# Kernel tuning notes

Measured on AMD Instinct MI355X. Metric: run time of the kernel, lower is better.

The kernel has to match this reference:

```python
import jax, jax.numpy as jnp
import numpy as np
import math

S, B, D = 1024, 8, 1024
H = 16
DK = D // H
F = 4096
EPS = 1e-5


def _layernorm(x, g, b):
    m = jnp.mean(x, axis=-1, keepdims=True)
    v = jnp.mean(jnp.square(x - m), axis=-1, keepdims=True)
    return (x - m) * jax.lax.rsqrt(v + EPS) * g + b


def setup_inputs() -> dict:
    key = jax.random.key(0)
    ks = jax.random.split(key, 16)
    sc = 0.02
    inp = {
        "src": jax.random.normal(ks[0], (S, B, D), dtype=jnp.float32),
        "pos": jax.random.normal(ks[1], (S, B, D), dtype=jnp.float32),
        "Wq": jax.random.normal(ks[2], (D, D), dtype=jnp.float32) * sc,
        "bq": jnp.zeros((D,), dtype=jnp.float32),
        "Wk": jax.random.normal(ks[3], (D, D), dtype=jnp.float32) * sc,
        "bk": jnp.zeros((D,), dtype=jnp.float32),
        "Wv": jax.random.normal(ks[4], (D, D), dtype=jnp.float32) * sc,
        "bv": jnp.zeros((D,), dtype=jnp.float32),
        "Wo": jax.random.normal(ks[5], (D, D), dtype=jnp.float32) * sc,
        "bo": jnp.zeros((D,), dtype=jnp.float32),
        "W1": jax.random.normal(ks[6], (D, F), dtype=jnp.float32) * sc,
        "b1": jnp.zeros((F,), dtype=jnp.float32),
        "W2": jax.random.normal(ks[7], (F, D), dtype=jnp.float32) * sc,
        "b2": jnp.zeros((D,), dtype=jnp.float32),
        "g1": jnp.ones((D,), dtype=jnp.float32),
        "be1": jnp.zeros((D,), dtype=jnp.float32),
        "g2": jnp.ones((D,), dtype=jnp.float32),
        "be2": jnp.zeros((D,), dtype=jnp.float32),
    }
    return inp


def reference(src, pos, Wq, bq, Wk, bk, Wv, bv, Wo, bo, W1, b1, W2, b2, g1, be1, g2, be2):
    # post-norm encoder layer; dropout = identity (eval mode)
    qk_in = src + pos                      # q = k = src + pos, value = src
    # to batch-first [B, S, D]
    qb = jnp.transpose(qk_in, (1, 0, 2))
    vb = jnp.transpose(src, (1, 0, 2))

    def split_heads(x):                    # [B,S,D] -> [B,H,S,DK]
        return jnp.transpose(x.reshape(B, S, H, DK), (0, 2, 1, 3))

    q = split_heads(qb @ Wq + bq)
    k = split_heads(qb @ Wk + bk)
    v = split_heads(vb @ Wv + bv)

    scores = jnp.einsum('bhqd,bhkd->bhqk', q, k) / math.sqrt(DK)
    attn = jax.nn.softmax(scores, axis=-1)             # [B,H,S,S]
    ctx = jnp.einsum('bhqk,bhkd->bhqd', attn, v)       # [B,H,S,DK]
    ctx = jnp.transpose(ctx, (0, 2, 1, 3)).reshape(B, S, D)
    attn_out = ctx @ Wo + bo                           # [B,S,D]
    attn_out = jnp.transpose(attn_out, (1, 0, 2))      # back to [S,B,D]

    x = _layernorm(src + attn_out, g1, be1)
    ffn = jax.nn.relu(x @ W1 + b1) @ W2 + b2
    out = _layernorm(x + ffn, g2, be2)
    return out, attn
```

## Files before the change

kernel.cpp:

```cpp
#include <hip/hip_runtime.h>
#include <stdint.h>

#define S_ 1024
#define B_ 8
#define D_ 1024
#define H_ 16
#define DK_ 64
#define F_ 4096
#define EPS_ 1e-5f

typedef __bf16 bf16_t;
typedef __attribute__((ext_vector_type(8))) __bf16 bf16x8;
typedef __attribute__((ext_vector_type(4))) __bf16 bf16x4;
typedef __attribute__((ext_vector_type(4))) float f32x4;

#define GLD16(gp, lp) __builtin_amdgcn_global_load_lds( \
    (__attribute__((address_space(1))) void*)(void*)(gp), \
    (__attribute__((address_space(3))) void*)(lp), 16, 0, 0)

#define BAR() __builtin_amdgcn_s_barrier()
#define SB0() __builtin_amdgcn_sched_barrier(0)
#define LG0() do { asm volatile("s_waitcnt lgkmcnt(0)" ::: "memory"); SB0(); } while (0)
#define VM6() asm volatile("s_waitcnt vmcnt(6)" ::: "memory")
#define VM4() asm volatile("s_waitcnt vmcnt(4)" ::: "memory")
#define VM3() asm volatile("s_waitcnt vmcnt(3)" ::: "memory")

template<int MODE>
__global__ __launch_bounds__(512, 2)
void gemm8p(const bf16_t* __restrict__ A, const bf16_t* __restrict__ Bt,
            const float* __restrict__ bias, const float* __restrict__ bias2,
            void* __restrict__ out, void* __restrict__ out2,
            int K, int lda, int ldb, int ldc)
{
    __shared__ __align__(16) bf16_t AsL[2][256][64];
    __shared__ __align__(16) bf16_t BsL[2][256][64];

    const int nwg = gridDim.x * gridDim.y;
    int flat = blockIdx.y * gridDim.x + blockIdx.x;
    flat = (flat & 7) * (nwg >> 3) + (flat >> 3);
    const int bx = flat % gridDim.x, by = flat / gridDim.x;
    const int rowBase = by * 256, colBase = bx * 256;

    const int tid = threadIdx.x;
    const int lane = tid & 63;
    const int wave = tid >> 6;
    const int wr = wave >> 2, wc = wave & 3;
    const int lr = lane & 15, quad = lane >> 4;

    const int r0 = tid >> 3, r1 = 64 + r0;
    const int cs = (tid & 7) ^ (r0 & 7);
    const int cl = tid & 7;
    const bf16_t* a0p = A + (size_t)(rowBase + r0) * lda + cs * 8;
    const bf16_t* a1p = A + (size_t)(rowBase + r1) * lda + cs * 8;
    const bf16_t* b0p = Bt + (size_t)(colBase + r0) * ldb + cs * 8;
    const bf16_t* b1p = Bt + (size_t)(colBase + r1) * ldb + cs * 8;

#define STAGE_A(buf, h, kel) do { \
    GLD16(a0p + (size_t)(h) * 128 * lda + (kel), &AsL[buf][(h) * 128 + r0][cl * 8]); \
    GLD16(a1p + (size_t)(h) * 128 * lda + (kel), &AsL[buf][(h) * 128 + r1][cl * 8]); } while (0)
#define STAGE_B(buf, h, kel) do { \
    GLD16(b0p + (size_t)(h) * 128 * ldb + (kel), &BsL[buf][(h) * 128 + r0][cl * 8]); \
    GLD16(b1p + (size_t)(h) * 128 * ldb + (kel), &BsL[buf][(h) * 128 + r1][cl * 8]); } while (0)

#define RDA(buf, qm, AF) do { \
    _Pragma("unroll") for (int mi = 0; mi < 4; ++mi) { \
        const int r_ = (qm) * 128 + wr * 64 + mi * 16 + lr; \
        _Pragma("unroll") for (int kk = 0; kk < 2; ++kk) \
            AF[mi * 2 + kk] = *(const bf16x8*)&AsL[buf][r_][((kk * 4 + quad) ^ (lr & 7)) * 8]; } } while (0)
#define RDB(buf, qn, BF) do { \
    _Pragma("unroll") for (int ni = 0; ni < 2; ++ni) { \
        const int r_ = (qn) * 128 + wc * 32 + ni * 16 + lr; \
        _Pragma("unroll") for (int kk = 0; kk < 2; ++kk) \
            BF[ni * 2 + kk] = *(const bf16x8*)&BsL[buf][r_][((kk * 4 + quad) ^ (lr & 7)) * 8]; } } while (0)

#define MQ(qm, qn, AF, BF) do { \
    __builtin_amdgcn_s_setprio(1); \
    _Pragma("unroll") for (int kk = 0; kk < 2; ++kk) \
    _Pragma("unroll") for (int mi = 0; mi < 4; ++mi) \
    _Pragma("unroll") for (int ni = 0; ni < 2; ++ni) \
        acc[(qm) * 4 + mi][(qn) * 2 + ni] = __builtin_amdgcn_mfma_f32_16x16x32_bf16( \
            AF[mi * 2 + kk], BF[ni * 2 + kk], acc[(qm) * 4 + mi][(qn) * 2 + ni], 0, 0, 0); \
    __builtin_amdgcn_s_setprio(0); } while (0)

    f32x4 acc[8][4] = {};
    bf16x8 af[8], bq0[4], bq1[4];

    STAGE_A(0, 0, 0); STAGE_B(0, 0, 0); STAGE_B(0, 1, 0); STAGE_A(0, 1, 0);
    STAGE_A(1, 0, 64); STAGE_B(1, 0, 64); STAGE_B(1, 1, 64);
    VM6();
    BAR(); SB0();

    const int NT = K >> 6;
    const int kCap = K - 64;
    for (int it = 0; it < (NT >> 1); ++it) {
        const int kP1 = it * 128 + 64;
        int kN0 = it * 128 + 128; if (kN0 > kCap) kN0 = kCap;
        int kN1 = it * 128 + 192; if (kN1 > kCap) kN1 = kCap;

        RDA(0, 0, af); RDB(0, 0, bq0);
        STAGE_A(1, 1, kP1);
        BAR(); LG0();
        MQ(0, 0, af, bq0);
        BAR(); SB0();
        RDB(0, 1, bq1);
        STAGE_A(0, 0, kN0);
        BAR(); LG0();
        MQ(0, 1, af, bq1);
        BAR(); SB0();
        RDA(0, 1, af);
        STAGE_B(0, 0, kN0);
        BAR(); LG0();
        MQ(1, 1, af, bq1);
        BAR(); SB0();
        STAGE_B(0, 1, kN0);
        BAR(); SB0();
        MQ(1, 0, af, bq0);
        VM6();
        BAR(); SB0();
        RDA(1, 0, af); RDB(1, 0, bq0);
        STAGE_A(0, 1, kN0);
        BAR(); LG0();
        MQ(0, 0, af, bq0);
        BAR(); SB0();
        RDB(1, 1, bq1);
        STAGE_A(1, 0, kN1);
        BAR(); LG0();
        MQ(0, 1, af, bq1);
        BAR(); SB0();
        RDA(1, 1, af);
        STAGE_B(1, 0, kN1);
        BAR(); LG0();
        MQ(1, 1, af, bq1);
        BAR(); SB0();
        STAGE_B(1, 1, kN1);
        BAR(); SB0();
        MQ(1, 0, af, bq0);
        VM6();
        BAR(); SB0();
    }

#pragma unroll
    for (int mi = 0; mi < 8; ++mi) {
#pragma unroll
        for (int ni = 0; ni < 4; ++ni) {
            const int col = colBase + (ni >> 1) * 128 + wc * 32 + (ni & 1) * 16 + lr;
            float bv;
            if constexpr (MODE == 0) bv = (col < 1024) ? bias[col] : bias2[col - 1024];
            else bv = bias[col];
#pragma unroll
            for (int e = 0; e < 4; ++e) {
                const int row = rowBase + (mi >> 2) * 128 + wr * 64 + (mi & 3) * 16 + quad * 4 + e;
                const float v = acc[mi][ni][e] + bv;
                if constexpr (MODE == 0) {
                    const int sel = col >> 10, c10 = col & 1023;
                    const int s = row >> 3, b = row & 7, h = c10 >> 6, dk = c10 & 63;
                    bf16_t* dst = sel ? (bf16_t*)out2 : (bf16_t*)out;
                    dst[(((size_t)(b * 16 + h) * 1024 + s) << 6) + dk] = (bf16_t)v;
                } else {
                    ((bf16_t*)out)[(size_t)row * ldc + col] = (bf16_t)fmaxf(v, 0.f);
                }
            }
        }
    }
#undef STAGE_A
#undef STAGE_B
#undef RDA
#undef RDB
#undef MQ
}

template<int MODE>
__global__ __launch_bounds__(512, 2)
void gemm4p(const bf16_t* __restrict__ A, const bf16_t* __restrict__ Bt,
            const float* __restrict__ bias, void* __restrict__ out,
            int K, int lda, int ldb, int ldc)
{
    __shared__ __align__(16) bf16_t AsL[2][256][64];
    __shared__ __align__(16) bf16_t BsL[2][128][64];

    const int nwg = gridDim.x * gridDim.y;
    int flat = blockIdx.y * gridDim.x + blockIdx.x;
    flat = (flat & 7) * (nwg >> 3) + (flat >> 3);
    const int bx = flat % gridDim.x, by = flat / gridDim.x;
    const int rowBase = by * 256, colBase = bx * 128;

    const int tid = threadIdx.x;
    const int lane = tid & 63;
    const int wave = tid >> 6;
    const int wr = wave >> 2, wc = wave & 3;
    const int lr = lane & 15, quad = lane >> 4;

    const int r0 = tid >> 3, r1 = 64 + r0;
    const int cs = (tid & 7) ^ (r0 & 7);
    const int cl = tid & 7;
    const bf16_t* a0p = A + (size_t)(rowBase + r0) * lda + cs * 8;
    const bf16_t* a1p = A + (size_t)(rowBase + r1) * lda + cs * 8;
    const bf16_t* b0p = Bt + (size_t)(colBase + r0) * ldb + cs * 8;

#define STAGE_A(buf, h, kel) do { \
    GLD16(a0p + (size_t)(h) * 128 * lda + (kel), &AsL[buf][(h) * 128 + r0][cl * 8]); \
    GLD16(a1p + (size_t)(h) * 128 * lda + (kel), &AsL[buf][(h) * 128 + r1][cl * 8]); } while (0)
#define STAGE_B(buf, h, kel) \
    GLD16(b0p + (size_t)(h) * 64 * ldb + (kel), &BsL[buf][(h) * 64 + r0][cl * 8])

#define RDA(buf, qm, AF) do { \
    _Pragma("unroll") for (int mi = 0; mi < 4; ++mi) { \
        const int r_ = (qm) * 128 + wr * 64 + mi * 16 + lr; \
        _Pragma("unroll") for (int kk = 0; kk < 2; ++kk) \
            AF[mi * 2 + kk] = *(const bf16x8*)&AsL[buf][r_][((kk * 4 + quad) ^ (lr & 7)) * 8]; } } while (0)
#define RDBF(buf, BQ) do { \
    _Pragma("unroll") for (int qn = 0; qn < 2; ++qn) { \
        const int r_ = qn * 64 + wc * 16 + lr; \
        _Pragma("unroll") for (int kk = 0; kk < 2; ++kk) \
            BQ[qn * 2 + kk] = *(const bf16x8*)&BsL[buf][r_][((kk * 4 + quad) ^ (lr & 7)) * 8]; } } while (0)

#define MQA(qm) do { \
    __builtin_amdgcn_s_setprio(1); \
    _Pragma("unroll") for (int kk = 0; kk < 2; ++kk) \
    _Pragma("unroll") for (int mi = 0; mi < 4; ++mi) \
    _Pragma("unroll") for (int qn = 0; qn < 2; ++qn) \
        acc[(qm) * 4 + mi][qn] = __builtin_amdgcn_mfma_f32_16x16x32_bf16( \
            af[mi * 2 + kk], bq[qn * 2 + kk], acc[(qm) * 4 + mi][qn], 0, 0, 0); \
    __builtin_amdgcn_s_setprio(0); } while (0)

    f32x4 acc[8][2] = {};
    bf16x8 af[8], bq[4];

    STAGE_A(0, 0, 0); STAGE_B(0, 0, 0); STAGE_B(0, 1, 0); STAGE_A(0, 1, 0);
    STAGE_A(1, 0, 64); STAGE_B(1, 0, 64); STAGE_B(1, 1, 64);
    VM4();
    BAR(); SB0();

    const int NT = K >> 6;
    const int kCap = K - 64;
    for (int it = 0; it < (NT >> 1); ++it) {
        const int kP1 = it * 128 + 64;
        int kN0 = it * 128 + 128; if (kN0 > kCap) kN0 = kCap;
        int kN1 = it * 128 + 192; if (kN1 > kCap) kN1 = kCap;

        RDA(0, 0, af); RDBF(0, bq);
        STAGE_A(1, 1, kP1);
        BAR(); LG0();
        MQA(0);
        BAR(); SB0();
        RDA(0, 1, af);
        STAGE_A(0, 0, kN0); STAGE_B(0, 0, kN0);
        BAR(); LG0();
        MQA(1);
        VM3();
        BAR(); SB0();
        RDA(1, 0, af); RDBF(1, bq);
        STAGE_B(0, 1, kN0); STAGE_A(0, 1, kN0);
        BAR(); LG0();
        MQA(0);
        BAR(); SB0();
        RDA(1, 1, af);
        STAGE_A(1, 0, kN1); STAGE_B(1, 0, kN1); STAGE_B(1, 1, kN1);
        BAR(); LG0();
        MQA(1);
        VM4();
        BAR(); SB0();
    }

#pragma unroll
    for (int mi = 0; mi < 8; ++mi) {
#pragma unroll
        for (int ni = 0; ni < 2; ++ni) {
            const int col = colBase + ni * 64 + wc * 16 + lr;
            const float bv = bias[col];
#pragma unroll
            for (int e = 0; e < 4; ++e) {
                const int row = rowBase + (mi >> 2) * 128 + wr * 64 + (mi & 3) * 16 + quad * 4 + e;
                const float v = acc[mi][ni][e] + bv;
                if constexpr (MODE == 0) {
                    ((float*)out)[(size_t)row * ldc + col] = v;
                } else {
                    const int s = row >> 3, b = row & 7, h = col >> 6, dk = col & 63;
                    ((bf16_t*)out)[(((size_t)(b * 16 + h) * 64 + dk) << 10) + s] = (bf16_t)v;
                }
            }
        }
    }
#undef STAGE_A
#undef STAGE_B
#undef RDA
#undef RDBF
#undef MQA
}

__global__ __launch_bounds__(256)
void fused_attn(const bf16_t* __restrict__ qb, const bf16_t* __restrict__ kb,
                const bf16_t* __restrict__ vt, float* __restrict__ attn,
                bf16_t* __restrict__ ctx)
{
    __shared__ __align__(16) bf16_t Psh[32 * 1024];
    __shared__ float smax[4][32];
    __shared__ float ssum[4][32];

    int flat = blockIdx.y * 32 + blockIdx.x;
    flat = (flat & 7) * 512 + (flat >> 3);
    const int z = flat >> 5;
    const int qBase = (flat & 31) * 32;
    const int b = z >> 4, h = z & 15;
    const int tid = threadIdx.x;
    const int wave = tid >> 6, lane = tid & 63;
    const int lr = lane & 15, quad = lane >> 4;

    const bf16_t* Qz = qb + ((size_t)z << 16);
    const bf16_t* Kz = kb + ((size_t)z << 16);
    const bf16_t* Vz = vt + ((size_t)z << 16);
    float* Az = attn + ((size_t)z << 20);

    bf16x8 qf[2][2];
#pragma unroll
    for (int ni = 0; ni < 2; ++ni)
#pragma unroll
        for (int kk = 0; kk < 2; ++kk)
            qf[ni][kk] = *(const bf16x8*)(Qz + (size_t)(qBase + ni * 16 + lr) * 64 + kk * 32 + quad * 8);

    f32x4 acc[16][2] = {};
#pragma unroll
    for (int mi = 0; mi < 16; ++mi) {
        const bf16_t* kp = Kz + (size_t)(wave * 256 + mi * 16 + lr) * 64 + quad * 8;
        bf16x8 kf0 = *(const bf16x8*)kp;
        bf16x8 kf1 = *(const bf16x8*)(kp + 32);
#pragma unroll
        for (int ni = 0; ni < 2; ++ni) {
            acc[mi][ni] = __builtin_amdgcn_mfma_f32_16x16x32_bf16(kf0, qf[ni][0], acc[mi][ni], 0, 0, 0);
            acc[mi][ni] = __builtin_amdgcn_mfma_f32_16x16x32_bf16(kf1, qf[ni][1], acc[mi][ni], 0, 0, 0);
        }
    }

    float mloc[2];
#pragma unroll
    for (int ni = 0; ni < 2; ++ni) {
        float mx = acc[0][ni][0];
#pragma unroll
        for (int mi = 0; mi < 16; ++mi)
            mx = fmaxf(mx, fmaxf(fmaxf(acc[mi][ni][0], acc[mi][ni][1]),
                                 fmaxf(acc[mi][ni][2], acc[mi][ni][3])));
        mx = fmaxf(mx, __shfl_xor(mx, 16, 64));
        mx = fmaxf(mx, __shfl_xor(mx, 32, 64));
        mloc[ni] = mx;
    }
    if (quad == 0) { smax[wave][lr] = mloc[0]; smax[wave][16 + lr] = mloc[1]; }
    __syncthreads();

    float rs[2];
#pragma unroll
    for (int ni = 0; ni < 2; ++ni) {
        const int qh = ni * 16 + lr;
        const float mm = 0.125f * fmaxf(fmaxf(smax[0][qh], smax[1][qh]),
                                        fmaxf(smax[2][qh], smax[3][qh]));
        float s = 0.f;
#pragma unroll
        for (int mi = 0; mi < 16; ++mi)
#pragma unroll
            for (int e = 0; e < 4; ++e) {
                float p = __expf(fmaf(acc[mi][ni][e], 0.125f, -mm));
                acc[mi][ni][e] = p; s += p;
            }
        s += __shfl_xor(s, 16, 64);
        s += __shfl_xor(s, 32, 64);
        rs[ni] = s;
    }
    if (quad == 0) { ssum[wave][lr] = rs[0]; ssum[wave][16 + lr] = rs[1]; }
    __syncthreads();

#pragma unroll
    for (int ni = 0; ni < 2; ++ni) {
        const int qh = ni * 16 + lr;
        const float r = 1.0f / (ssum[0][qh] + ssum[1][qh] + ssum[2][qh] + ssum[3][qh]);
        float* arow = Az + ((size_t)(qBase + qh) << 10);
#pragma unroll
        for (int mi = 0; mi < 16; ++mi) {
            const int k0 = wave * 256 + mi * 16 + quad * 4;
            f32x4 o;
            o[0] = acc[mi][ni][0] * r; o[1] = acc[mi][ni][1] * r;
            o[2] = acc[mi][ni][2] * r; o[3] = acc[mi][ni][3] * r;
            __builtin_nontemporal_store(o, (f32x4*)(arow + k0));
            bf16x4 pb;
            pb[0] = (bf16_t)o[0]; pb[1] = (bf16_t)o[1]; pb[2] = (bf16_t)o[2]; pb[3] = (bf16_t)o[3];
            int byte = qh * 2048 + k0 * 2;
            byte ^= (qh & 7) << 4;
            *(bf16x4*)((char*)Psh + byte) = pb;
        }
    }
    __syncthreads();

    f32x4 cacc[2] = {};
#pragma unroll
    for (int kt = 0; kt < 32; ++kt) {
        bf16x8 vf = *(const bf16x8*)(Vz + (size_t)(wave * 16 + lr) * 1024 + kt * 32 + quad * 8);
#pragma unroll
        for (int mi = 0; mi < 2; ++mi) {
            const int qh = mi * 16 + lr;
            int byte = qh * 2048 + (kt * 32 + quad * 8) * 2;
            byte ^= (qh & 7) << 4;
            bf16x8 af = *(const bf16x8*)((const char*)Psh + byte);
            cacc[mi] = __builtin_amdgcn_mfma_f32_16x16x32_bf16(af, vf, cacc[mi], 0, 0, 0);
        }
    }
#pragma unroll
    for (int mi = 0; mi < 2; ++mi)
#pragma unroll
        for (int e = 0; e < 4; ++e) {
            const int s = qBase + mi * 16 + quad * 4 + e;
            ctx[(((size_t)s * 8 + b) << 10) + h * 64 + wave * 16 + lr] = (bf16_t)cacc[mi][e];
        }
}

__global__ __launch_bounds__(256)
void prep_kernel(const float* __restrict__ src, const float* __restrict__ pos,
                 bf16_t* __restrict__ qk, bf16_t* __restrict__ vv)
{
    const size_t i = ((size_t)blockIdx.x * 256 + threadIdx.x) * 4;
    float4 s = *(const float4*)(src + i);
    float4 q = *(const float4*)(pos + i);
    bf16x4 qo, vo;
    qo[0] = (bf16_t)(s.x + q.x); qo[1] = (bf16_t)(s.y + q.y);
    qo[2] = (bf16_t)(s.z + q.z); qo[3] = (bf16_t)(s.w + q.w);
    vo[0] = (bf16_t)s.x; vo[1] = (bf16_t)s.y; vo[2] = (bf16_t)s.z; vo[3] = (bf16_t)s.w;
    *(bf16x4*)(qk + i) = qo;
    *(bf16x4*)(vv + i) = vo;
}

__global__ __launch_bounds__(256)
void transpose_w4(const float* __restrict__ W0, const float* __restrict__ W1,
                  const float* __restrict__ W2, const float* __restrict__ W3,
                  bf16_t* __restrict__ T0, bf16_t* __restrict__ T1,
                  bf16_t* __restrict__ T2, bf16_t* __restrict__ T3)
{
    __shared__ float t[32][33];
    const float* W; bf16_t* T;
    switch (blockIdx.z) {
        case 0: W = W0; T = T0; break;
        case 1: W = W1; T = T1; break;
        case 2: W = W2; T = T2; break;
        default: W = W3; T = T3; break;
    }
    const int n0 = blockIdx.x * 32, k0 = blockIdx.y * 32;
    const int tx = threadIdx.x & 31;
    const int ty = threadIdx.x >> 5;
#pragma unroll
    for (int j = 0; j < 32; j += 8)
        t[ty + j][tx] = W[(size_t)(k0 + ty + j) * 1024 + n0 + tx];
    __syncthreads();
#pragma unroll
    for (int j = 0; j < 32; j += 8)
        T[(size_t)(n0 + ty + j) * 1024 + k0 + tx] = (bf16_t)t[tx][ty + j];
}

__global__ __launch_bounds__(256)
void transpose_w(const float* __restrict__ W, bf16_t* __restrict__ WT, int K, int N)
{
    __shared__ float t[32][33];
    const int n0 = blockIdx.x * 32, k0 = blockIdx.y * 32;
    const int tx = threadIdx.x & 31;
    const int ty = threadIdx.x >> 5;
#pragma unroll
    for (int j = 0; j < 32; j += 8)
        t[ty + j][tx] = W[(size_t)(k0 + ty + j) * N + n0 + tx];
    __syncthreads();
#pragma unroll
    for (int j = 0; j < 32; j += 8)
        WT[(size_t)(n0 + ty + j) * K + k0 + tx] = (bf16_t)t[tx][ty + j];
}

__global__ __launch_bounds__(256)
void ln_kernel(const float* __restrict__ a, const float* __restrict__ b,
               const float* __restrict__ g, const float* __restrict__ be,
               float* __restrict__ xf, bf16_t* __restrict__ xb, float* __restrict__ outf)
{
    __shared__ float sh[8];
    const int r = blockIdx.x;
    const int t = threadIdx.x;
    float4 va = ((const float4*)(a + ((size_t)r << 10)))[t];
    float4 vb = ((const float4*)(b + ((size_t)r << 10)))[t];
    float x0 = va.x + vb.x, x1 = va.y + vb.y, x2 = va.z + vb.z, x3 = va.w + vb.w;
    float s = x0 + x1 + x2 + x3;
    float sq = x0 * x0 + x1 * x1 + x2 * x2 + x3 * x3;
#pragma unroll
    for (int o = 32; o > 0; o >>= 1) { s += __shfl_xor(s, o, 64); sq += __shfl_xor(sq, o, 64); }
    const int w = t >> 6, ln = t & 63;
    if (ln == 0) { sh[w] = s; sh[4 + w] = sq; }
    __syncthreads();
    s = sh[0] + sh[1] + sh[2] + sh[3];
    sq = sh[4] + sh[5] + sh[6] + sh[7];
    const float mean = s * (1.f / 1024.f);
    const float var = sq * (1.f / 1024.f) - mean * mean;
    const float rstd = rsqrtf(var + EPS_);
    float4 vg = ((const float4*)g)[t];
    float4 vbe = ((const float4*)be)[t];
    float y0 = (x0 - mean) * rstd * vg.x + vbe.x;
    float y1 = (x1 - mean) * rstd * vg.y + vbe.y;
    float y2 = (x2 - mean) * rstd * vg.z + vbe.z;
    float y3 = (x3 - mean) * rstd * vg.w + vbe.w;
    if (xf) { float4 o4 = {y0, y1, y2, y3}; ((float4*)(xf + ((size_t)r << 10)))[t] = o4; }
    if (xb) {
        bf16x4 ob; ob[0] = (bf16_t)y0; ob[1] = (bf16_t)y1; ob[2] = (bf16_t)y2; ob[3] = (bf16_t)y3;
        ((bf16x4*)(xb + ((size_t)r << 10)))[t] = ob;
    }
    if (outf) { float4 o4 = {y0, y1, y2, y3}; ((float4*)(outf + ((size_t)r << 10)))[t] = o4; }
}

extern "C" void kernel_launch(void* const* d_in, const int* in_sizes, int n_in,
                              void* d_out, int out_size, void* d_ws, size_t ws_size,
                              hipStream_t stream)
{
    (void)in_sizes; (void)n_in; (void)out_size; (void)ws_size;
    const float* src = (const float*)d_in[0];
    const float* pos = (const float*)d_in[1];
    const float* Wq  = (const float*)d_in[2];
    const float* bq  = (const float*)d_in[3];
    const float* Wk  = (const float*)d_in[4];
    const float* bk  = (const float*)d_in[5];
    const float* Wv  = (const float*)d_in[6];
    const float* bv  = (const float*)d_in[7];
    const float* Wo  = (const float*)d_in[8];
    const float* bo  = (const float*)d_in[9];
    const float* W1  = (const float*)d_in[10];
    const float* b1  = (const float*)d_in[11];
    const float* W2  = (const float*)d_in[12];
    const float* b2  = (const float*)d_in[13];
    const float* g1  = (const float*)d_in[14];
    const float* be1 = (const float*)d_in[15];
    const float* g2  = (const float*)d_in[16];
    const float* be2 = (const float*)d_in[17];

    float* outF  = (float*)d_out;
    float* attnF = outF + (size_t)S_ * B_ * D_;

    char* ws = (char*)d_ws;
    size_t off = 0;
    auto alloc = [&](size_t bytes) { void* p = ws + off; off += (bytes + 255) & ~(size_t)255; return p; };

    bf16_t* qk_bf = (bf16_t*)alloc((size_t)8192 * 1024 * 2);
    bf16_t* v_bf  = (bf16_t*)alloc((size_t)8192 * 1024 * 2);
    bf16_t* wqT   = (bf16_t*)alloc((size_t)1024 * 1024 * 2);
    bf16_t* wkT   = (bf16_t*)alloc((size_t)1024 * 1024 * 2);
    bf16_t* wvT   = (bf16_t*)alloc((size_t)1024 * 1024 * 2);
    bf16_t* woT   = (bf16_t*)alloc((size_t)1024 * 1024 * 2);
    bf16_t* w1T   = (bf16_t*)alloc((size_t)4096 * 1024 * 2);
    bf16_t* w2T   = (bf16_t*)alloc((size_t)1024 * 4096 * 2);
    bf16_t* qbuf  = (bf16_t*)alloc((size_t)8 * 16 * 1024 * 64 * 2);
    bf16_t* kbuf  = (bf16_t*)alloc((size_t)8 * 16 * 1024 * 64 * 2);
    bf16_t* vtbuf = (bf16_t*)alloc((size_t)8 * 16 * 64 * 1024 * 2);
    bf16_t* ctx_bf= (bf16_t*)alloc((size_t)8192 * 1024 * 2);
    float*  ao_f  = (float*)alloc((size_t)8192 * 1024 * 4);
    float*  x_f   = (float*)alloc((size_t)8192 * 1024 * 4);
    bf16_t* x_bf  = (bf16_t*)alloc((size_t)8192 * 1024 * 2);
    bf16_t* h_bf  = (bf16_t*)alloc((size_t)8192 * 4096 * 2);
    float*  y_f   = (float*)alloc((size_t)8192 * 1024 * 4);

    transpose_w4<<<dim3(32, 32, 4), 256, 0, stream>>>(Wq, Wk, Wv, Wo, wqT, wkT, wvT, woT);
    transpose_w<<<dim3(128, 32), 256, 0, stream>>>(W1, w1T, 1024, 4096);
    transpose_w<<<dim3(32, 128), 256, 0, stream>>>(W2, w2T, 4096, 1024);

    prep_kernel<<<8192, 256, 0, stream>>>(src, pos, qk_bf, v_bf);

    gemm8p<0><<<dim3(8, 32), 512, 0, stream>>>(qk_bf, wqT, bq, bk, qbuf, kbuf, 1024, 1024, 1024, 0);
    gemm4p<2><<<dim3(8, 32), 512, 0, stream>>>(v_bf, wvT, bv, vtbuf, 1024, 1024, 1024, 0);

    fused_attn<<<dim3(32, 128), 256, 0, stream>>>(qbuf, kbuf, vtbuf, attnF, ctx_bf);

    gemm4p<0><<<dim3(8, 32), 512, 0, stream>>>(ctx_bf, woT, bo, ao_f, 1024, 1024, 1024, 1024);

    ln_kernel<<<8192, 256, 0, stream>>>(src, ao_f, g1, be1, x_f, x_bf, nullptr);

    gemm8p<1><<<dim3(16, 32), 512, 0, stream>>>(x_bf, w1T, b1, nullptr, h_bf, nullptr, 1024, 1024, 1024, 4096);
    gemm4p<0><<<dim3(8, 32), 512, 0, stream>>>(h_bf, w2T, b2, y_f, 4096, 4096, 4096, 1024);

    ln_kernel<<<8192, 256, 0, stream>>>(x_f, y_f, g2, be2, nullptr, nullptr, outF);
}
```

Before: 564.2 us.

## Split-K the FFN down-projection with gemm8p and reduce partials in layernorm

The W2 GEMM (K=4096, N=1024) moves from gemm4p to the larger-tile gemm8p kernel with a two-way split along K via blockIdx.z. Each half writes fp32 partial sums to its own buffer, and bias is added only by the first split. The final layernorm kernel now reads and sums the second partial, and it writes the output with nontemporal stores. This trades extra fp32 partial-sum traffic (another 32MB written and read) for a 256-wide N tile and a 4x32x2 grid that keeps the GPU occupied.

```diff
diff --git a/kernel.cpp b/kernel.cpp
--- a/kernel.cpp
+++ b/kernel.cpp
@@ -30,10 +30,15 @@
 void gemm8p(const bf16_t* __restrict__ A, const bf16_t* __restrict__ Bt,
             const float* __restrict__ bias, const float* __restrict__ bias2,
             void* __restrict__ out, void* __restrict__ out2,
-            int K, int lda, int ldb, int ldc)
+            int K, int lda, int ldb, int ldc,
+            long zA, long zB, long zC)
 {
     __shared__ __align__(16) bf16_t AsL[2][256][64];
     __shared__ __align__(16) bf16_t BsL[2][256][64];
+
+    const int zi = blockIdx.z;
+    A += (size_t)zi * zA;
+    Bt += (size_t)zi * zB;
 
     const int nwg = gridDim.x * gridDim.y;
     int flat = blockIdx.y * gridDim.x + blockIdx.x;
@@ -146,6 +151,7 @@
             const int col = colBase + (ni >> 1) * 128 + wc * 32 + (ni & 1) * 16 + lr;
             float bv;
             if constexpr (MODE == 0) bv = (col < 1024) ? bias[col] : bias2[col - 1024];
+            else if constexpr (MODE == 2) bv = zi ? 0.f : bias[col];
             else bv = bias[col];
 #pragma unroll
             for (int e = 0; e < 4; ++e) {
@@ -156,8 +162,10 @@
                     const int s = row >> 3, b = row & 7, h = c10 >> 6, dk = c10 & 63;
                     bf16_t* dst = sel ? (bf16_t*)out2 : (bf16_t*)out;
                     dst[(((size_t)(b * 16 + h) * 1024 + s) << 6) + dk] = (bf16_t)v;
+                } else if constexpr (MODE == 1) {
+                    ((bf16_t*)out)[(size_t)row * ldc + col] = (bf16_t)fmaxf(v, 0.f);
                 } else {
-                    ((bf16_t*)out)[(size_t)row * ldc + col] = (bf16_t)fmaxf(v, 0.f);
+                    ((float*)out)[(size_t)zi * zC + (size_t)row * ldc + col] = v;
                 }
             }
         }
@@ -469,6 +477,7 @@
 
 __global__ __launch_bounds__(256)
 void ln_kernel(const float* __restrict__ a, const float* __restrict__ b,
+               const float* __restrict__ b2,
                const float* __restrict__ g, const float* __restrict__ be,
                float* __restrict__ xf, bf16_t* __restrict__ xb, float* __restrict__ outf)
 {
@@ -478,6 +487,10 @@
     float4 va = ((const float4*)(a + ((size_t)r << 10)))[t];
     float4 vb = ((const float4*)(b + ((size_t)r << 10)))[t];
     float x0 = va.x + vb.x, x1 = va.y + vb.y, x2 = va.z + vb.z, x3 = va.w + vb.w;
+    if (b2) {
+        float4 vc = ((const float4*)(b2 + ((size_t)r << 10)))[t];
+        x0 += vc.x; x1 += vc.y; x2 += vc.z; x3 += vc.w;
+    }
     float s = x0 + x1 + x2 + x3;
     float sq = x0 * x0 + x1 * x1 + x2 * x2 + x3 * x3;
 #pragma unroll
@@ -501,7 +514,10 @@
         bf16x4 ob; ob[0] = (bf16_t)y0; ob[1] = (bf16_t)y1; ob[2] = (bf16_t)y2; ob[3] = (bf16_t)y3;
         ((bf16x4*)(xb + ((size_t)r << 10)))[t] = ob;
     }
-    if (outf) { float4 o4 = {y0, y1, y2, y3}; ((float4*)(outf + ((size_t)r << 10)))[t] = o4; }
+    if (outf) {
+        f32x4 o4 = {y0, y1, y2, y3};
+        __builtin_nontemporal_store(o4, (f32x4*)(outf + ((size_t)r << 10)) + t);
+    }
 }
 
 extern "C" void kernel_launch(void* const* d_in, const int* in_sizes, int n_in,
@@ -551,7 +567,7 @@
     float*  x_f   = (float*)alloc((size_t)8192 * 1024 * 4);
     bf16_t* x_bf  = (bf16_t*)alloc((size_t)8192 * 1024 * 2);
     bf16_t* h_bf  = (bf16_t*)alloc((size_t)8192 * 4096 * 2);
-    float*  y_f   = (float*)alloc((size_t)8192 * 1024 * 4);
+    float*  y_f   = (float*)alloc((size_t)8192 * 1024 * 4 * 2);
 
     transpose_w4<<<dim3(32, 32, 4), 256, 0, stream>>>(Wq, Wk, Wv, Wo, wqT, wkT, wvT, woT);
     transpose_w<<<dim3(128, 32), 256, 0, stream>>>(W1, w1T, 1024, 4096);
@@ -559,17 +575,19 @@
 
     prep_kernel<<<8192, 256, 0, stream>>>(src, pos, qk_bf, v_bf);
 
-    gemm8p<0><<<dim3(8, 32), 512, 0, stream>>>(qk_bf, wqT, bq, bk, qbuf, kbuf, 1024, 1024, 1024, 0);
+    gemm8p<0><<<dim3(8, 32, 1), 512, 0, stream>>>(qk_bf, wqT, bq, bk, qbuf, kbuf, 1024, 1024, 1024, 0, 0, 0, 0);
     gemm4p<2><<<dim3(8, 32), 512, 0, stream>>>(v_bf, wvT, bv, vtbuf, 1024, 1024, 1024, 0);
 
     fused_attn<<<dim3(32, 128), 256, 0, stream>>>(qbuf, kbuf, vtbuf, attnF, ctx_bf);
 
     gemm4p<0><<<dim3(8, 32), 512, 0, stream>>>(ctx_bf, woT, bo, ao_f, 1024, 1024, 1024, 1024);
 
-    ln_kernel<<<8192, 256, 0, stream>>>(src, ao_f, g1, be1, x_f, x_bf, nullptr);
-
-    gemm8p<1><<<dim3(16, 32), 512, 0, stream>>>(x_bf, w1T, b1, nullptr, h_bf, nullptr, 1024, 1024, 1024, 4096);
-    gemm4p<0><<<dim3(8, 32), 512, 0, stream>>>(h_bf, w2T, b2, y_f, 4096, 4096, 4096, 1024);
-
-    ln_kernel<<<8192, 256, 0, stream>>>(x_f, y_f, g2, be2, nullptr, nullptr, outF);
-}
+    ln_kernel<<<8192, 256, 0, stream>>>(src, ao_f, nullptr, g1, be1, x_f, x_bf, nullptr);
+
+    gemm8p<1><<<dim3(16, 32, 1), 512, 0, stream>>>(x_bf, w1T, b1, nullptr, h_bf, nullptr, 1024, 1024, 1024, 4096, 0, 0, 0);
+    gemm8p<2><<<dim3(4, 32, 2), 512, 0, stream>>>(h_bf, w2T, b2, nullptr, y_f, nullptr,
+                                                  2048, 4096, 4096, 1024,
+                                                  2048, 2048, (long)8192 * 1024);
+
+    ln_kernel<<<8192, 256, 0, stream>>>(x_f, y_f, y_f + (size_t)8192 * 1024, g2, be2, nullptr, nullptr, outF);
+}
```

Measured after the change: 565.8 us. Within noise of the previous version (+0.3%).
